# Optimization experiments

Measured on AMD Instinct MI355X. Metric: run time of the kernel, lower is better.

## Reference

```python
import jax, jax.numpy as jnp
import numpy as np

N = 50000    # nodes
E = 800000   # edges
G = 128      # graphs in batch
IN = 128     # in_dim
H = 4        # num_heads
D = 32       # hidden_dim (per head)
C = 10       # n_classes
NEG_SLOPE = 0.2  # DGL GATConv default


def setup_inputs() -> dict:
    key = jax.random.key(0)
    ks = jax.random.split(key, 14)
    def winit(k, shape, fan_in):
        return jax.random.normal(k, shape, jnp.float32) / np.float32(np.sqrt(fan_in))
    h = jax.random.normal(ks[0], (N, IN), jnp.float32)
    src = jax.random.randint(ks[1], (E,), 0, N)
    dst = jax.random.randint(ks[2], (E,), 0, N)
    graph_id = jnp.sort(jax.random.randint(ks[3], (N,), 0, G))
    # GATConv layer 1: fc weight, attention vectors a_l/a_r, output bias
    W1 = winit(ks[4], (IN, H * D), IN)
    al1 = winit(ks[5], (H, D), D)
    ar1 = winit(ks[6], (H, D), D)
    b1 = jnp.zeros((H, D), jnp.float32)
    # GATConv layer 2 (input width H*D)
    W2 = winit(ks[7], (H * D, H * D), H * D)
    al2 = winit(ks[8], (H, D), D)
    ar2 = winit(ks[9], (H, D), D)
    b2 = jnp.zeros((H, D), jnp.float32)
    # classifier
    Wc = winit(ks[10], (H * D, C), H * D)
    bc = jnp.zeros((C,), jnp.float32)
    return dict(h=h, src=src, dst=dst, graph_id=graph_id,
                W1=W1, al1=al1, ar1=ar1, b1=b1,
                W2=W2, al2=al2, ar2=ar2, b2=b2, Wc=Wc, bc=bc)


def gat_layer(h, W, al, ar, b, src, dst):
    # h: [N, F_in] -> z: [N, H, D]
    z = (h @ W).reshape(-1, H, D)
    el = jnp.einsum('nhd,hd->nh', z, al)   # src-side attention logits
    er = jnp.einsum('nhd,hd->nh', z, ar)   # dst-side attention logits
    e = jax.nn.leaky_relu(el[src] + er[dst], NEG_SLOPE)  # [E, H]
    # edge softmax over incoming edges of each destination node
    emax = jax.lax.stop_gradient(jax.ops.segment_max(e, dst, num_segments=N))
    ee = jnp.exp(e - emax[dst])
    denom = jax.ops.segment_sum(ee, dst, num_segments=N)
    alpha = ee / denom[dst]                # [E, H]
    out = jax.ops.segment_sum(z[src] * alpha[:, :, None], dst, num_segments=N)
    return out + b                         # [N, H, D]


def reference(h, src, dst, graph_id, W1, al1, ar1, b1, W2, al2, ar2, b2, Wc, bc):
    x = jax.nn.relu(gat_layer(h, W1, al1, ar1, b1, src, dst)).reshape(N, H * D)
    x = jax.nn.relu(gat_layer(x, W2, al2, ar2, b2, src, dst)).reshape(N, H * D)
    sums = jax.ops.segment_sum(x, graph_id, num_segments=G)          # [G, H*D]
    counts = jax.ops.segment_sum(jnp.ones((N, 1), x.dtype), graph_id, num_segments=G)
    hg = sums / jnp.maximum(counts, 1.0)   # mean_nodes
    return hg @ Wc + bc                    # [G, C]
```

## Files before the change

kernel.cpp:

```cpp
#include <hip/hip_runtime.h>
#include <hip/hip_fp16.h>
#include <math.h>

#define NN 50000
#define NE 800000
#define NG 128
#define HD 128
#define NH 4
#define NC 10
#define NEG_SLOPE 0.2f

typedef _Float16 f16x8 __attribute__((ext_vector_type(8)));
typedef float    f32x4 __attribute__((ext_vector_type(4)));

#define GROWS 64
__global__ __launch_bounds__(256, 2) void k_gemm_attn(
    const float* __restrict__ X, const float* __restrict__ W,
    const float* __restrict__ al, const float* __restrict__ ar,
    __half* __restrict__ Zh, float* __restrict__ el, float* __restrict__ er)
{
    __shared__ __align__(16) _Float16 Wp[4][8][64][8];
    const int tid = threadIdx.x;
    for (int idx = tid; idx < 128 * 32; idx += 256) {
        int k = idx >> 5, n4 = idx & 31;
        float4 wv = *(const float4*)&W[k * HD + n4 * 4];
        int kt = k >> 5, kin = k & 31;
        int kg = kin >> 3, j = kin & 7;
        #pragma unroll
        for (int q = 0; q < 4; ++q) {
            int n = n4 * 4 + q;
            float v = (q == 0) ? wv.x : (q == 1) ? wv.y : (q == 2) ? wv.z : wv.w;
            Wp[kt][n >> 4][kg * 16 + (n & 15)][j] = (_Float16)v;
        }
    }
    const int w = tid >> 6, l = tid & 63;
    const int l15 = l & 15, lg = l >> 4;
    const int rbase = blockIdx.x * GROWS + w * 16;
    int arow = rbase + l15;
    int arow_c = arow < NN ? arow : NN - 1;
    __syncthreads();

    f32x4 acc[8];
    #pragma unroll
    for (int nt = 0; nt < 8; ++nt) acc[nt] = (f32x4)(0.f);

    #pragma unroll
    for (int kt = 0; kt < 4; ++kt) {
        const float* xp = &X[(size_t)arow_c * HD + kt * 32 + lg * 8];
        float4 x0 = *(const float4*)xp;
        float4 x1 = *(const float4*)(xp + 4);
        f16x8 afrag;
        afrag[0] = (_Float16)x0.x; afrag[1] = (_Float16)x0.y;
        afrag[2] = (_Float16)x0.z; afrag[3] = (_Float16)x0.w;
        afrag[4] = (_Float16)x1.x; afrag[5] = (_Float16)x1.y;
        afrag[6] = (_Float16)x1.z; afrag[7] = (_Float16)x1.w;
        #pragma unroll
        for (int nt = 0; nt < 8; ++nt) {
            f16x8 bfrag = *(const f16x8*)&Wp[kt][nt][l][0];
            acc[nt] = __builtin_amdgcn_mfma_f32_16x16x32_f16(afrag, bfrag, acc[nt], 0, 0, 0);
        }
    }

    float alv[8], arv[8];
    #pragma unroll
    for (int nt = 0; nt < 8; ++nt) {
        alv[nt] = al[nt * 16 + l15];
        arv[nt] = ar[nt * 16 + l15];
    }
    float pl[4][4], pr[4][4];
    #pragma unroll
    for (int j = 0; j < 4; ++j)
        #pragma unroll
        for (int h = 0; h < 4; ++h) {
            pl[j][h] = acc[2*h][j] * alv[2*h] + acc[2*h+1][j] * alv[2*h+1];
            pr[j][h] = acc[2*h][j] * arv[2*h] + acc[2*h+1][j] * arv[2*h+1];
        }
    #pragma unroll
    for (int off = 1; off <= 8; off <<= 1)
        #pragma unroll
        for (int j = 0; j < 4; ++j)
            #pragma unroll
            for (int h = 0; h < 4; ++h) {
                pl[j][h] += __shfl_xor(pl[j][h], off);
                pr[j][h] += __shfl_xor(pr[j][h], off);
            }
    if (l15 == 0) {
        #pragma unroll
        for (int j = 0; j < 4; ++j) {
            int r = rbase + lg * 4 + j;
            if (r < NN) {
                *(float4*)&el[(size_t)r * NH] = make_float4(pl[j][0], pl[j][1], pl[j][2], pl[j][3]);
                *(float4*)&er[(size_t)r * NH] = make_float4(pr[j][0], pr[j][1], pr[j][2], pr[j][3]);
            }
        }
    }
    #pragma unroll
    for (int j = 0; j < 4; ++j) {
        int r = rbase + lg * 4 + j;
        if (r < NN) {
            #pragma unroll
            for (int nt = 0; nt < 8; ++nt)
                Zh[(size_t)r * HD + nt * 16 + l15] = __float2half(acc[nt][j]);
        }
    }
}

__global__ void k_deg(const int* __restrict__ dst, int* __restrict__ deg,
                      int* __restrict__ rank) {
    int t = blockIdx.x * blockDim.x + threadIdx.x;
    if (t < NE) rank[t] = atomicAdd(&deg[dst[t]], 1);
}

#define SCAN_B 1024
#define NBLK ((NN + SCAN_B - 1) / SCAN_B)

__global__ __launch_bounds__(1024) void k_scan1(const int* __restrict__ deg,
                                                int* __restrict__ offs,
                                                int* __restrict__ bsum)
{
    __shared__ int wsum[16];
    const int tid = threadIdx.x, lane = tid & 63, w = tid >> 6;
    const int i = blockIdx.x * SCAN_B + tid;
    int v = (i < NN) ? deg[i] : 0;
    int x = v;
    #pragma unroll
    for (int off = 1; off < 64; off <<= 1) {
        int t = __shfl_up(x, off);
        if (lane >= off) x += t;
    }
    if (lane == 63) wsum[w] = x;
    __syncthreads();
    if (w == 0 && lane < 16) {
        int t = wsum[lane];
        #pragma unroll
        for (int off = 1; off < 16; off <<= 1) {
            int u = __shfl_up(t, off);
            if (lane >= off) t += u;
        }
        wsum[lane] = t;
    }
    __syncthreads();
    int wbase = (w == 0) ? 0 : wsum[w - 1];
    if (i < NN) offs[i] = wbase + x - v;
    if (tid == 0) bsum[blockIdx.x] = wsum[15];
}

__global__ __launch_bounds__(64) void k_scan2(int* __restrict__ bsum,
                                              int* __restrict__ offs)
{
    const int lane = threadIdx.x;
    int v = (lane < NBLK) ? bsum[lane] : 0;
    int x = v;
    #pragma unroll
    for (int off = 1; off < 64; off <<= 1) {
        int t = __shfl_up(x, off);
        if (lane >= off) x += t;
    }
    if (lane < NBLK) bsum[lane] = x - v;
    if (lane == 63) offs[NN] = x;
}

__global__ __launch_bounds__(1024) void k_scan3(int* __restrict__ offs,
                                                const int* __restrict__ bsum)
{
    const int i = blockIdx.x * SCAN_B + threadIdx.x;
    if (i < NN) offs[i] += bsum[blockIdx.x];
}

__global__ void k_scatter(const int* __restrict__ src, const int* __restrict__ dst,
                          const int* __restrict__ rank, const int* __restrict__ offs,
                          int* __restrict__ csrc) {
    int t = blockIdx.x * blockDim.x + threadIdx.x;
    if (t < NE) {
        csrc[offs[dst[t]] + rank[t]] = src[t];
    }
}

__global__ __launch_bounds__(256) void k_edge_gat(
    const int* __restrict__ offs, const int* __restrict__ csrc,
    const float* __restrict__ el, const float* __restrict__ er,
    const __half* __restrict__ Zh, const float* __restrict__ b,
    float* __restrict__ X)
{
    int wid = (int)((blockIdx.x * (unsigned)blockDim.x + threadIdx.x) >> 6);
    int lane = threadIdx.x & 63;
    if (wid >= NN) return;
    const int d = wid;
    const int beg = offs[d], end = offs[d + 1];
    const int c0 = lane * 2;
    const int h = lane >> 4;
    const float erd = er[d * NH + h];
    const float2 bb = *(const float2*)&b[c0];

    float s0 = 0.f, s1 = 0.f;
    float a0x = 0.f, a0y = 0.f, a1x = 0.f, a1y = 0.f;
    int i = beg;
    for (; i + 3 < end; i += 4) {
        int sA = csrc[i], sB = csrc[i + 1], sC = csrc[i + 2], sD = csrc[i + 3];
        __half2 zA = *(const __half2*)&Zh[(size_t)sA * HD + c0];
        __half2 zB = *(const __half2*)&Zh[(size_t)sB * HD + c0];
        __half2 zC = *(const __half2*)&Zh[(size_t)sC * HD + c0];
        __half2 zD = *(const __half2*)&Zh[(size_t)sD * HD + c0];
        float eA = el[sA * NH + h] + erd;
        float eB = el[sB * NH + h] + erd;
        float eC = el[sC * NH + h] + erd;
        float eD = el[sD * NH + h] + erd;
        eA = eA >= 0.f ? eA : NEG_SLOPE * eA;
        eB = eB >= 0.f ? eB : NEG_SLOPE * eB;
        eC = eC >= 0.f ? eC : NEG_SLOPE * eC;
        eD = eD >= 0.f ? eD : NEG_SLOPE * eD;
        float pA = __expf(eA), pB = __expf(eB), pC = __expf(eC), pD = __expf(eD);
        float2 fA = __half22float2(zA);
        float2 fB = __half22float2(zB);
        float2 fC = __half22float2(zC);
        float2 fD = __half22float2(zD);
        s0 += pA + pB;
        s1 += pC + pD;
        a0x = fmaf(fA.x, pA, a0x); a0y = fmaf(fA.y, pA, a0y);
        a1x = fmaf(fB.x, pB, a1x); a1y = fmaf(fB.y, pB, a1y);
        a0x = fmaf(fC.x, pC, a0x); a0y = fmaf(fC.y, pC, a0y);
        a1x = fmaf(fD.x, pD, a1x); a1y = fmaf(fD.y, pD, a1y);
    }
    for (; i < end; ++i) {
        int s = csrc[i];
        __half2 zh = *(const __half2*)&Zh[(size_t)s * HD + c0];
        float e = el[s * NH + h] + erd;
        e = e >= 0.f ? e : NEG_SLOPE * e;
        float p = __expf(e);
        float2 f = __half22float2(zh);
        s0 += p;
        a0x = fmaf(f.x, p, a0x);
        a0y = fmaf(f.y, p, a0y);
    }
    float sden = s0 + s1;
    float ax = a0x + a1x, ay = a0y + a1y;
    float inv = (end > beg) ? 1.f / sden : 0.f;
    float v0 = ax * inv + bb.x;
    float v1 = ay * inv + bb.y;
    float2 o;
    o.x = v0 > 0.f ? v0 : 0.f;
    o.y = v1 > 0.f ? v1 : 0.f;
    *(float2*)&X[(size_t)d * HD + c0] = o;
}

__global__ __launch_bounds__(1024) void k_pool_classify(
    const float* __restrict__ X, const int* __restrict__ gid,
    const float* __restrict__ Wc, const float* __restrict__ bc,
    float* __restrict__ out)
{
    __shared__ float part[8][HD];
    __shared__ float shg[HD];
    __shared__ int slo, shi;
    const int g = blockIdx.x;
    const int tid = threadIdx.x;
    const int c = tid & 127;
    const int gr = tid >> 7;
    if (tid == 0) {
        int lo = 0, hi = NN;
        while (lo < hi) { int mid = (lo + hi) >> 1; if (gid[mid] < g) lo = mid + 1; else hi = mid; }
        slo = lo;
        int lo2 = lo; hi = NN;
        while (lo2 < hi) { int mid = (lo2 + hi) >> 1; if (gid[mid] < g + 1) lo2 = mid + 1; else hi = mid; }
        shi = lo2;
    }
    __syncthreads();
    const int lo = slo, hi = shi;
    float acc = 0.f;
    for (int n = lo + gr; n < hi; n += 8) acc += X[(size_t)n * HD + c];
    part[gr][c] = acc;
    __syncthreads();
    if (gr == 0) {
        float s = part[0][c] + part[1][c] + part[2][c] + part[3][c]
                + part[4][c] + part[5][c] + part[6][c] + part[7][c];
        shg[c] = s / fmaxf((float)(hi - lo), 1.f);
    }
    __syncthreads();
    if (tid < NC) {
        float r = bc[tid];
        #pragma unroll
        for (int k = 0; k < HD; ++k) r = fmaf(shg[k], Wc[k * NC + tid], r);
        out[g * NC + tid] = r;
    }
}

extern "C" void kernel_launch(void* const* d_in, const int* in_sizes, int n_in,
                              void* d_out, int out_size, void* d_ws, size_t ws_size,
                              hipStream_t stream) {
    const float* h    = (const float*)d_in[0];
    const int*   src  = (const int*)  d_in[1];
    const int*   dst  = (const int*)  d_in[2];
    const int*   gid  = (const int*)  d_in[3];
    const float* W1   = (const float*)d_in[4];
    const float* al1  = (const float*)d_in[5];
    const float* ar1  = (const float*)d_in[6];
    const float* b1   = (const float*)d_in[7];
    const float* W2   = (const float*)d_in[8];
    const float* al2  = (const float*)d_in[9];
    const float* ar2  = (const float*)d_in[10];
    const float* b2   = (const float*)d_in[11];
    const float* Wc   = (const float*)d_in[12];
    const float* bc   = (const float*)d_in[13];
    float* out = (float*)d_out;

    char* w = (char*)d_ws;
    __half* zh  = (__half*)w; w += (size_t)NN * HD * 2;
    float* xb   = (float*)w;  w += (size_t)NN * HD * 4;
    float* el   = (float*)w;  w += (size_t)NN * NH * 4;
    float* er   = (float*)w;  w += (size_t)NN * NH * 4;
    int*   deg  = (int*)w;    w += (size_t)NN * 4;
    int*   offs = (int*)w;    w += (size_t)(NN + 1) * 4;
    int*   bsum = (int*)w;    w += (size_t)NBLK * 4;
    int*   rank = (int*)w;    w += (size_t)NE * 4;
    int*   csrc = (int*)w;    w += (size_t)NE * 4;

    const int TB = 256;
    const int gE    = (NE + TB - 1) / TB;
    const int gGemm = (NN + GROWS - 1) / GROWS;
    const int gEdge = (NN * 64 + TB - 1) / TB;

    hipMemsetAsync(deg, 0, (size_t)NN * 4, stream);
    k_deg<<<gE, TB, 0, stream>>>(dst, deg, rank);
    k_scan1<<<NBLK, SCAN_B, 0, stream>>>(deg, offs, bsum);
    k_scan2<<<1, 64, 0, stream>>>(bsum, offs);
    k_scan3<<<NBLK, SCAN_B, 0, stream>>>(offs, bsum);
    k_scatter<<<gE, TB, 0, stream>>>(src, dst, rank, offs, csrc);

    k_gemm_attn<<<gGemm, 256, 0, stream>>>(h, W1, al1, ar1, zh, el, er);
    k_edge_gat<<<gEdge, TB, 0, stream>>>(offs, csrc, el, er, zh, b1, xb);

    k_gemm_attn<<<gGemm, 256, 0, stream>>>(xb, W2, al2, ar2, zh, el, er);
    k_edge_gat<<<gEdge, TB, 0, stream>>>(offs, csrc, el, er, zh, b2, xb);

    k_pool_classify<<<NG, 1024, 0, stream>>>(xb, gid, Wc, bc, out);
}
```

Baseline: 303.5 us.

## Process four destination nodes per wave in edge aggregation and vectorize CSR build

The edge aggregation kernel now gives each destination node 16 lanes instead of a full 64-lane wave. Each lane loads 8 fp16 features with a 16-byte load and accumulates them, with the edge loop unrolled by two. This raises memory-level parallelism per wave and reduces per-node index/logit loads, which matters because average degree is around 16. The degree-count and scatter kernels also process four edges per thread using int4 loads. The cost is more divergence across nodes of unequal degree within a wave and shorter unroll depth.

```diff
diff --git a/kernel.cpp b/kernel.cpp
--- a/kernel.cpp
+++ b/kernel.cpp
@@ -107,8 +107,18 @@
 
 __global__ void k_deg(const int* __restrict__ dst, int* __restrict__ deg,
                       int* __restrict__ rank) {
-    int t = blockIdx.x * blockDim.x + threadIdx.x;
-    if (t < NE) rank[t] = atomicAdd(&deg[dst[t]], 1);
+    int base = (blockIdx.x * blockDim.x + threadIdx.x) * 4;
+    if (base + 3 < NE) {
+        int4 d4 = *(const int4*)&dst[base];
+        int4 r4;
+        r4.x = atomicAdd(&deg[d4.x], 1);
+        r4.y = atomicAdd(&deg[d4.y], 1);
+        r4.z = atomicAdd(&deg[d4.z], 1);
+        r4.w = atomicAdd(&deg[d4.w], 1);
+        *(int4*)&rank[base] = r4;
+    } else {
+        for (int t = base; t < NE; ++t) rank[t] = atomicAdd(&deg[dst[t]], 1);
+    }
 }
 
 #define SCAN_B 1024
@@ -170,9 +180,17 @@
 __global__ void k_scatter(const int* __restrict__ src, const int* __restrict__ dst,
                           const int* __restrict__ rank, const int* __restrict__ offs,
                           int* __restrict__ csrc) {
-    int t = blockIdx.x * blockDim.x + threadIdx.x;
-    if (t < NE) {
-        csrc[offs[dst[t]] + rank[t]] = src[t];
+    int base = (blockIdx.x * blockDim.x + threadIdx.x) * 4;
+    if (base + 3 < NE) {
+        int4 s4 = *(const int4*)&src[base];
+        int4 d4 = *(const int4*)&dst[base];
+        int4 r4 = *(const int4*)&rank[base];
+        csrc[offs[d4.x] + r4.x] = s4.x;
+        csrc[offs[d4.y] + r4.y] = s4.y;
+        csrc[offs[d4.z] + r4.z] = s4.z;
+        csrc[offs[d4.w] + r4.w] = s4.w;
+    } else {
+        for (int t = base; t < NE; ++t) csrc[offs[dst[t]] + rank[t]] = src[t];
     }
 }
 
@@ -182,65 +200,83 @@
     const __half* __restrict__ Zh, const float* __restrict__ b,
     float* __restrict__ X)
 {
-    int wid = (int)((blockIdx.x * (unsigned)blockDim.x + threadIdx.x) >> 6);
+    int wave = (int)((blockIdx.x * (unsigned)blockDim.x + threadIdx.x) >> 6);
     int lane = threadIdx.x & 63;
-    if (wid >= NN) return;
-    const int d = wid;
+    int sub = lane >> 4;
+    int hl  = lane & 15;
+    int d = wave * 4 + sub;
+    if (d >= NN) return;
     const int beg = offs[d], end = offs[d + 1];
-    const int c0 = lane * 2;
-    const int h = lane >> 4;
+    const int c0 = hl * 8;
+    const int h = hl >> 2;
     const float erd = er[d * NH + h];
-    const float2 bb = *(const float2*)&b[c0];
-
-    float s0 = 0.f, s1 = 0.f;
-    float a0x = 0.f, a0y = 0.f, a1x = 0.f, a1y = 0.f;
+    const float4 bb0 = *(const float4*)&b[c0];
+    const float4 bb1 = *(const float4*)&b[c0 + 4];
+
+    float sden = 0.f;
+    float a0 = 0.f, a1 = 0.f, a2 = 0.f, a3 = 0.f;
+    float a4 = 0.f, a5 = 0.f, a6 = 0.f, a7 = 0.f;
+
     int i = beg;
-    for (; i + 3 < end; i += 4) {
-        int sA = csrc[i], sB = csrc[i + 1], sC = csrc[i + 2], sD = csrc[i + 3];
-        __half2 zA = *(const __half2*)&Zh[(size_t)sA * HD + c0];
-        __half2 zB = *(const __half2*)&Zh[(size_t)sB * HD + c0];
-        __half2 zC = *(const __half2*)&Zh[(size_t)sC * HD + c0];
-        __half2 zD = *(const __half2*)&Zh[(size_t)sD * HD + c0];
+    for (; i + 1 < end; i += 2) {
+        int sA = csrc[i], sB = csrc[i + 1];
+        uint4 uA = *(const uint4*)&Zh[(size_t)sA * HD + c0];
+        uint4 uB = *(const uint4*)&Zh[(size_t)sB * HD + c0];
         float eA = el[sA * NH + h] + erd;
         float eB = el[sB * NH + h] + erd;
-        float eC = el[sC * NH + h] + erd;
-        float eD = el[sD * NH + h] + erd;
         eA = eA >= 0.f ? eA : NEG_SLOPE * eA;
         eB = eB >= 0.f ? eB : NEG_SLOPE * eB;
-        eC = eC >= 0.f ? eC : NEG_SLOPE * eC;
-        eD = eD >= 0.f ? eD : NEG_SLOPE * eD;
-        float pA = __expf(eA), pB = __expf(eB), pC = __expf(eC), pD = __expf(eD);
-        float2 fA = __half22float2(zA);
-        float2 fB = __half22float2(zB);
-        float2 fC = __half22float2(zC);
-        float2 fD = __half22float2(zD);
-        s0 += pA + pB;
-        s1 += pC + pD;
-        a0x = fmaf(fA.x, pA, a0x); a0y = fmaf(fA.y, pA, a0y);
-        a1x = fmaf(fB.x, pB, a1x); a1y = fmaf(fB.y, pB, a1y);
-        a0x = fmaf(fC.x, pC, a0x); a0y = fmaf(fC.y, pC, a0y);
-        a1x = fmaf(fD.x, pD, a1x); a1y = fmaf(fD.y, pD, a1y);
-    }
-    for (; i < end; ++i) {
+        float pA = __expf(eA), pB = __expf(eB);
+        sden += pA + pB;
+        {
+            float2 f0 = __half22float2(*(const __half2*)&uA.x);
+            float2 f1 = __half22float2(*(const __half2*)&uA.y);
+            float2 f2 = __half22float2(*(const __half2*)&uA.z);
+            float2 f3 = __half22float2(*(const __half2*)&uA.w);
+            a0 = fmaf(f0.x, pA, a0); a1 = fmaf(f0.y, pA, a1);
+            a2 = fmaf(f1.x, pA, a2); a3 = fmaf(f1.y, pA, a3);
+            a4 = fmaf(f2.x, pA, a4); a5 = fmaf(f2.y, pA, a5);
+            a6 = fmaf(f3.x, pA, a6); a7 = fmaf(f3.y, pA, a7);
+        }
+        {
+            float2 f0 = __half22float2(*(const __half2*)&uB.x);
+            float2 f1 = __half22float2(*(const __half2*)&uB.y);
+            float2 f2 = __half22float2(*(const __half2*)&uB.z);
+            float2 f3 = __half22float2(*(const __half2*)&uB.w);
+            a0 = fmaf(f0.x, pB, a0); a1 = fmaf(f0.y, pB, a1);
+            a2 = fmaf(f1.x, pB, a2); a3 = fmaf(f1.y, pB, a3);
+            a4 = fmaf(f2.x, pB, a4); a5 = fmaf(f2.y, pB, a5);
+            a6 = fmaf(f3.x, pB, a6); a7 = fmaf(f3.y, pB, a7);
+        }
+    }
+    if (i < end) {
         int s = csrc[i];
-        __half2 zh = *(const __half2*)&Zh[(size_t)s * HD + c0];
+        uint4 u = *(const uint4*)&Zh[(size_t)s * HD + c0];
         float e = el[s * NH + h] + erd;
         e = e >= 0.f ? e : NEG_SLOPE * e;
         float p = __expf(e);
-        float2 f = __half22float2(zh);
-        s0 += p;
-        a0x = fmaf(f.x, p, a0x);
-        a0y = fmaf(f.y, p, a0y);
-    }
-    float sden = s0 + s1;
-    float ax = a0x + a1x, ay = a0y + a1y;
+        sden += p;
+        float2 f0 = __half22float2(*(const __half2*)&u.x);
+        float2 f1 = __half22float2(*(const __half2*)&u.y);
+        float2 f2 = __half22float2(*(const __half2*)&u.z);
+        float2 f3 = __half22float2(*(const __half2*)&u.w);
+        a0 = fmaf(f0.x, p, a0); a1 = fmaf(f0.y, p, a1);
+        a2 = fmaf(f1.x, p, a2); a3 = fmaf(f1.y, p, a3);
+        a4 = fmaf(f2.x, p, a4); a5 = fmaf(f2.y, p, a5);
+        a6 = fmaf(f3.x, p, a6); a7 = fmaf(f3.y, p, a7);
+    }
     float inv = (end > beg) ? 1.f / sden : 0.f;
-    float v0 = ax * inv + bb.x;
-    float v1 = ay * inv + bb.y;
-    float2 o;
-    o.x = v0 > 0.f ? v0 : 0.f;
-    o.y = v1 > 0.f ? v1 : 0.f;
-    *(float2*)&X[(size_t)d * HD + c0] = o;
+    float4 o0, o1;
+    o0.x = fmaxf(fmaf(a0, inv, bb0.x), 0.f);
+    o0.y = fmaxf(fmaf(a1, inv, bb0.y), 0.f);
+    o0.z = fmaxf(fmaf(a2, inv, bb0.z), 0.f);
+    o0.w = fmaxf(fmaf(a3, inv, bb0.w), 0.f);
+    o1.x = fmaxf(fmaf(a4, inv, bb1.x), 0.f);
+    o1.y = fmaxf(fmaf(a5, inv, bb1.y), 0.f);
+    o1.z = fmaxf(fmaf(a6, inv, bb1.z), 0.f);
+    o1.w = fmaxf(fmaf(a7, inv, bb1.w), 0.f);
+    *(float4*)&X[(size_t)d * HD + c0]     = o0;
+    *(float4*)&X[(size_t)d * HD + c0 + 4] = o1;
 }
 
 __global__ __launch_bounds__(1024) void k_pool_classify(
@@ -314,16 +350,16 @@
     int*   csrc = (int*)w;    w += (size_t)NE * 4;
 
     const int TB = 256;
-    const int gE    = (NE + TB - 1) / TB;
+    const int gE4   = (NE / 4 + TB - 1) / TB;
     const int gGemm = (NN + GROWS - 1) / GROWS;
-    const int gEdge = (NN * 64 + TB - 1) / TB;
+    const int gEdge = ((NN + 3) / 4 * 64 + TB - 1) / TB;
 
     hipMemsetAsync(deg, 0, (size_t)NN * 4, stream);
-    k_deg<<<gE, TB, 0, stream>>>(dst, deg, rank);
+    k_deg<<<gE4, TB, 0, stream>>>(dst, deg, rank);
     k_scan1<<<NBLK, SCAN_B, 0, stream>>>(deg, offs, bsum);
     k_scan2<<<1, 64, 0, stream>>>(bsum, offs);
     k_scan3<<<NBLK, SCAN_B, 0, stream>>>(offs, bsum);
-    k_scatter<<<gE, TB, 0, stream>>>(src, dst, rank, offs, csrc);
+    k_scatter<<<gE4, TB, 0, stream>>>(src, dst, rank, offs, csrc);
 
     k_gemm_attn<<<gGemm, 256, 0, stream>>>(h, W1, al1, ar1, zh, el, er);
     k_edge_gat<<<gEdge, TB, 0, stream>>>(offs, csrc, el, er, zh, b1, xb);
```

Result: faster. 289.1 us (-4.8%).
